# Kernel optimization log

Hardware: AMD Instinct MI355X
Metric: run time of the kernel (lower is better)

## Reference

```python
import jax, jax.numpy as jnp
import numpy as np


def _gru(x, w_ih, w_hh, b_ih, b_hh, reverse=False):
    # PyTorch GRU cell math. x: (N, T, Din) -> (N, T, Hh)
    N, T, _ = x.shape
    Hh = w_hh.shape[1]
    xp = jnp.einsum('ntd,gd->ntg', x, w_ih) + b_ih  # (N, T, 3*Hh), input gates precomputed

    def step(h, xp_t):
        gh = h @ w_hh.T + b_hh
        ir, iz, inn = jnp.split(xp_t, 3, axis=-1)
        hr, hz, hn = jnp.split(gh, 3, axis=-1)
        r = jax.nn.sigmoid(ir + hr)
        z = jax.nn.sigmoid(iz + hz)
        n = jnp.tanh(inn + r * hn)
        h_new = (1.0 - z) * n + z * h
        return h_new, h_new

    h0 = jnp.zeros((N, Hh), x.dtype)
    _, ys = jax.lax.scan(step, h0, jnp.swapaxes(xp, 0, 1), reverse=reverse)
    return jnp.swapaxes(ys, 0, 1)


def _bigru(x, pf, pb):
    return jnp.concatenate([_gru(x, *pf), _gru(x, *pb, reverse=True)], axis=-1)


def _attn(out, w, b, ctx):
    # out: (N, T, H). tanh(Linear) -> context dot -> softmax -> weighted sum
    u = jnp.tanh(jnp.einsum('nth,gh->ntg', out, w) + b)
    a = jax.nn.softmax(u @ ctx, axis=-1)  # (N, T)
    return jnp.einsum('nt,nth->nh', a, out)


def setup_inputs() -> dict:
    key = jax.random.key(0)
    H, Hh = 512, 256
    S, B, Nsent = 2048, 16, 16
    L = S // Nsent
    ks = jax.random.split(key, 32)

    def p(k, shape):
        return jax.random.normal(k, shape, jnp.float32) * 0.05

    starts = jnp.arange(Nsent, dtype=jnp.int32) * L
    spans = jnp.stack([starts, starts + L], axis=-1)  # (Nsent, 2)
    spans = jnp.broadcast_to(spans, (B, Nsent, 2))

    inp = {
        'token_feats': jax.random.normal(ks[0], (S, B, H), jnp.float32),
        'sentence_spans': spans,
        # word BiGRU params (forward / backward directions)
        'w_wih_f': p(ks[1], (3 * Hh, H)), 'w_whh_f': p(ks[2], (3 * Hh, Hh)),
        'w_bih_f': p(ks[3], (3 * Hh,)), 'w_bhh_f': p(ks[4], (3 * Hh,)),
        'w_wih_b': p(ks[5], (3 * Hh, H)), 'w_whh_b': p(ks[6], (3 * Hh, Hh)),
        'w_bih_b': p(ks[7], (3 * Hh,)), 'w_bhh_b': p(ks[8], (3 * Hh,)),
        # sentence BiGRU params
        's_wih_f': p(ks[9], (3 * Hh, H)), 's_whh_f': p(ks[10], (3 * Hh, Hh)),
        's_bih_f': p(ks[11], (3 * Hh,)), 's_bhh_f': p(ks[12], (3 * Hh,)),
        's_wih_b': p(ks[13], (3 * Hh, H)), 's_whh_b': p(ks[14], (3 * Hh, Hh)),
        's_bih_b': p(ks[15], (3 * Hh,)), 's_bhh_b': p(ks[16], (3 * Hh,)),
        # attention params
        'w_attn_w': p(ks[17], (H, H)), 'w_attn_b': p(ks[18], (H,)),
        'w_ctx': jax.random.normal(ks[19], (H,), jnp.float32),
        's_attn_w': p(ks[20], (H, H)), 's_attn_b': p(ks[21], (H,)),
        's_ctx': jax.random.normal(ks[22], (H,), jnp.float32),
    }
    return inp


def reference(token_feats, sentence_spans,
              w_wih_f, w_whh_f, w_bih_f, w_bhh_f,
              w_wih_b, w_whh_b, w_bih_b, w_bhh_b,
              s_wih_f, s_whh_f, s_bih_f, s_bhh_f,
              s_wih_b, s_whh_b, s_bih_b, s_bhh_b,
              w_attn_w, w_attn_b, w_ctx,
              s_attn_w, s_attn_b, s_ctx):
    S, B, H = token_feats.shape
    Nsent = sentence_spans.shape[1]
    L = S // Nsent  # uniform spans: segment b,i = tokens [i*L, (i+1)*L)

    x = jnp.swapaxes(token_feats, 0, 1)  # (B, S, H)
    segs = x.reshape(B * Nsent, L, H)    # all sentences batched together

    # word-level BiGRU + word attention -> sentence vectors
    out_w = _bigru(segs, (w_wih_f, w_whh_f, w_bih_f, w_bhh_f),
                   (w_wih_b, w_whh_b, w_bih_b, w_bhh_b))  # (B*Nsent, L, H)
    sent_vecs = _attn(out_w, w_attn_w, w_attn_b, w_ctx).reshape(B, Nsent, H)

    # sentence-level BiGRU + sentence attention (no padding: all masks true)
    out_s = _bigru(sent_vecs, (s_wih_f, s_whh_f, s_bih_f, s_bhh_f),
                   (s_wih_b, s_whh_b, s_bih_b, s_bhh_b))  # (B, Nsent, H)
    Yh = _attn(out_s, s_attn_w, s_attn_b, s_ctx)  # (B, H)
    return Yh
```

## Files before the change

kernel.cpp:

```cpp
#include <hip/hip_runtime.h>
#include <stdint.h>


using uint32  = unsigned int;
using bf16x8  = __attribute__((ext_vector_type(8))) __bf16;
using floatx4 = __attribute__((ext_vector_type(4))) float;

__device__ __forceinline__ float b2f(unsigned short u) {
    union { uint32 i; float f; } v; v.i = ((uint32)u) << 16; return v.f;
}
__device__ __forceinline__ unsigned short f2b(float f) {
    union { float f; uint32 i; } v; v.f = f;
    uint32 r = v.i + 0x7fffu + ((v.i >> 16) & 1u);
    return (unsigned short)(r >> 16);
}
__device__ __forceinline__ float sigmoidf_(float x) { return 1.f / (1.f + __expf(-x)); }
__device__ __forceinline__ float tanhf_(float x) {
    x = fminf(15.f, fmaxf(-15.f, x));
    float e = __expf(2.f * x);
    return (e - 1.f) / (e + 1.f);
}

__device__ __forceinline__ void gl16(const unsigned short* g, unsigned short* l) {
    __builtin_amdgcn_global_load_lds(
        (const __attribute__((address_space(1))) uint32*)g,
        (__attribute__((address_space(3))) uint32*)l, 16, 0, 0);
}

__device__ __forceinline__ void bar_lgkm() {
    asm volatile("s_waitcnt lgkmcnt(0)");
    __builtin_amdgcn_sched_barrier(0);
    __builtin_amdgcn_s_barrier();
    __builtin_amdgcn_sched_barrier(0);
}

#define O_XPC     0L
#define O_OWHI    50331648L
#define O_OWLO    83886080L
#define O_STATE   117440512L
#define O_SCW     117964800L
#define O_W0HI    118095872L
#define O_W0LO    118882304L
#define O_W1HI    119668736L
#define O_W1LO    120455168L
#define O_WAHI    121241600L
#define O_WALO    121765888L
#define O_S0HI    122290176L
#define O_S0LO    123076608L
#define O_S1HI    123863040L
#define O_S1LO    124649472L
#define O_SAHI    125435904L
#define O_SALO    125960192L
#define O_HW0     126484480L
#define O_HW1     126877696L
#define O_HS0     127270912L
#define O_HS1     127664128L
#define O_SENTHI  128057344L
#define O_SENTLO  128319488L
#define O_XPS     128581632L
#define O_SSTATE  130154496L
#define O_OSHI    130187264L
#define O_OSLO    130449408L
#define O_SCS     130711552L
#define O_TKWH    130712576L
#define O_TKWL    164267008L

__global__ __launch_bounds__(256)
void cvt_hilo6(const float* __restrict__ s0, const float* __restrict__ s1,
               const float* __restrict__ s2, const float* __restrict__ s3,
               const float* __restrict__ s4, const float* __restrict__ s5,
               char* __restrict__ ws)
{
    const int b = blockIdx.x;
    const float* src; unsigned short *hi, *lo; int base;
    if (b < 192)      { src = s0; hi = (unsigned short*)(ws + O_W0HI); lo = (unsigned short*)(ws + O_W0LO); base = b; }
    else if (b < 384) { src = s1; hi = (unsigned short*)(ws + O_W1HI); lo = (unsigned short*)(ws + O_W1LO); base = b - 192; }
    else if (b < 576) { src = s2; hi = (unsigned short*)(ws + O_S0HI); lo = (unsigned short*)(ws + O_S0LO); base = b - 384; }
    else if (b < 768) { src = s3; hi = (unsigned short*)(ws + O_S1HI); lo = (unsigned short*)(ws + O_S1LO); base = b - 576; }
    else if (b < 896) { src = s4; hi = (unsigned short*)(ws + O_WAHI); lo = (unsigned short*)(ws + O_WALO); base = b - 768; }
    else              { src = s5; hi = (unsigned short*)(ws + O_SAHI); lo = (unsigned short*)(ws + O_SALO); base = b - 896; }
    const int idx = (base * 256 + threadIdx.x) * 8;
    float f[8];
    *reinterpret_cast<float4*>(&f[0]) = *reinterpret_cast<const float4*>(src + idx);
    *reinterpret_cast<float4*>(&f[4]) = *reinterpret_cast<const float4*>(src + idx + 4);
    unsigned short h[8], l[8];
    #pragma unroll
    for (int j = 0; j < 8; ++j) {
        h[j] = f2b(f[j]);
        l[j] = f2b(f[j] - b2f(h[j]));
    }
    *reinterpret_cast<uint4*>(hi + idx) = *reinterpret_cast<const uint4*>(h);
    *reinterpret_cast<uint4*>(lo + idx) = *reinterpret_cast<const uint4*>(l);
}

__global__ __launch_bounds__(256)
void cvt_b4(const float* __restrict__ s0, const float* __restrict__ s1,
            const float* __restrict__ s2, const float* __restrict__ s3,
            char* __restrict__ ws)
{
    const int b = blockIdx.x;
    const float* src; unsigned short* dst; int base;
    if (b < 96)       { src = s0; dst = (unsigned short*)(ws + O_HW0); base = b; }
    else if (b < 192) { src = s1; dst = (unsigned short*)(ws + O_HW1); base = b - 96; }
    else if (b < 288) { src = s2; dst = (unsigned short*)(ws + O_HS0); base = b - 192; }
    else              { src = s3; dst = (unsigned short*)(ws + O_HS1); base = b - 288; }
    const int idx = (base * 256 + threadIdx.x) * 8;
    float f[8];
    *reinterpret_cast<float4*>(&f[0]) = *reinterpret_cast<const float4*>(src + idx);
    *reinterpret_cast<float4*>(&f[4]) = *reinterpret_cast<const float4*>(src + idx + 4);
    unsigned short o[8];
    #pragma unroll
    for (int j = 0; j < 8; ++j) o[j] = f2b(f[j]);
    *reinterpret_cast<uint4*>(dst + idx) = *reinterpret_cast<const uint4*>(o);
}

__global__ __launch_bounds__(256)
void cvt_tokfull(const float* __restrict__ tok, unsigned short* __restrict__ whi,
                 unsigned short* __restrict__ wlo)
{
    const int u = blockIdx.x * 256 + threadIdx.x;
    const int h8 = u & 63;
    const int rest = u >> 6;
    const int t = rest & 127, seq = rest >> 7;
    const int sent = seq & 15, b = seq >> 4;
    const long src = ((long)(sent * 128 + t) * 16 + b) * 512 + h8 * 8;
    float f[8];
    *reinterpret_cast<float4*>(&f[0]) = *reinterpret_cast<const float4*>(tok + src);
    *reinterpret_cast<float4*>(&f[4]) = *reinterpret_cast<const float4*>(tok + src + 4);
    unsigned short h[8], l[8];
    #pragma unroll
    for (int j = 0; j < 8; ++j) {
        h[j] = f2b(f[j]);
        l[j] = f2b(f[j] - b2f(h[j]));
    }
    const long dst = (long)rest * 512 + h8 * 8;
    *reinterpret_cast<uint4*>(whi + dst) = *reinterpret_cast<const uint4*>(h);
    *reinterpret_cast<uint4*>(wlo + dst) = *reinterpret_cast<const uint4*>(l);
}

template<int AMODE>
__device__ __forceinline__ long amap(int m, int t0, int sgn) {
    if (AMODE == 1) {
        const int sq = m >> 5, tl = m & 31;
        return (long)(sq * 128 + t0 + sgn * tl) * 512;
    } else if (AMODE == 3) {
        const int n = m >> 4, tl = m & 15;
        return (long)(n * 16 + t0 + sgn * tl) * 512;
    }
    return (long)m * 512;
}

template<int AMODE, int OUT>
__global__ __launch_bounds__(512, 2)
void gemm_t(const unsigned short* __restrict__ Ahi, const unsigned short* __restrict__ Alo,
            const unsigned short* __restrict__ Wh0, const unsigned short* __restrict__ Wl0,
            const unsigned short* __restrict__ Wh1, const unsigned short* __restrict__ Wl1,
            const float* __restrict__ b0, const float* __restrict__ b1,
            float* __restrict__ C, int ldC, long c1off,
            float* __restrict__ score, const float* __restrict__ ctx,
            int t00, int t01, int nbyHalf)
{
    __shared__ __align__(16) unsigned short smem[2 * 32768];

    int bx = blockIdx.x, by = blockIdx.y;
    {
        const int nbx = gridDim.x, nby = gridDim.y;
        if ((nby & 7) == 0) {
            const int l = by * nbx + bx;
            const int xcd = l & 7;
            const int s = l >> 3;
            bx = s % nbx;
            by = xcd * (nby >> 3) + s / nbx;
        }
    }

    const int tid  = threadIdx.x;
    const int lane = tid & 63;
    const int wave = tid >> 6;
    const int wm = wave >> 2, wn = wave & 3;
    const int n_base = bx * 256;
    const int q = lane >> 4;
    const int r = lane & 15;

    const unsigned short* Whi = Wh0;
    const unsigned short* Wlo = Wl0;
    const float* bias = b0;
    float* Cb = C;
    int t0 = t00, sgn = 1, m_base;
    if (nbyHalf > 0 && by >= nbyHalf) {
        Whi = Wh1; Wlo = Wl1; bias = b1; Cb = C + c1off;
        t0 = t01; sgn = -1;
        m_base = (by - nbyHalf) * 256;
    } else {
        m_base = by * 256;
    }

    long aoff[2], woff[2];
    #pragma unroll
    for (int i = 0; i < 2; ++i) {
        const int s = tid + 512 * i;
        const int R = s >> 2, kg = s & 3;
        const int kq = (kg - (R >> 1)) & 3;
        aoff[i] = amap<AMODE>(m_base + R, t0, sgn) + kq * 8;
        woff[i] = (long)(n_base + R) * 512 + kq * 8;
    }

    floatx4 acc[8][4];
    #pragma unroll
    for (int mt = 0; mt < 8; ++mt)
        #pragma unroll
        for (int nt = 0; nt < 4; ++nt) acc[mt][nt] = (floatx4){0.f, 0.f, 0.f, 0.f};

    auto stage = [&](int ts) {
        const int k0 = ts * 32;
        unsigned short* B = smem + (ts & 1) * 32768;
        #pragma unroll
        for (int i = 0; i < 2; ++i) {
            const int ld = (tid + 512 * i) * 8;
            gl16(Ahi + aoff[i] + k0, B + ld);
            gl16(Alo + aoff[i] + k0, B + 8192 + ld);
            gl16(Whi + woff[i] + k0, B + 16384 + ld);
            gl16(Wlo + woff[i] + k0, B + 24576 + ld);
        }
    };

    stage(0);
    asm volatile("s_waitcnt vmcnt(0)");
    __builtin_amdgcn_sched_barrier(0);
    __builtin_amdgcn_s_barrier();
    __builtin_amdgcn_sched_barrier(0);

    for (int t = 0; t < 16; ++t) {
        if (t + 1 < 16) stage(t + 1);

        const unsigned short* B   = smem + (t & 1) * 32768;
        const unsigned short* BAl = B + 8192;
        const unsigned short* BW  = B + 16384;
        const unsigned short* BWl = B + 24576;

        bf16x8 wh[4], wl[4], ah[8], al[8];
        #pragma unroll
        for (int nt = 0; nt < 4; ++nt) {
            const int Rn = wn * 64 + nt * 16 + r;
            const int sn = Rn * 4 + ((q + (Rn >> 1)) & 3);
            wh[nt] = *reinterpret_cast<const bf16x8*>(BW  + sn * 8);
            wl[nt] = *reinterpret_cast<const bf16x8*>(BWl + sn * 8);
        }
        #pragma unroll
        for (int mt = 0; mt < 8; ++mt) {
            const int R = wm * 128 + mt * 16 + r;
            const int s = R * 4 + ((q + (R >> 1)) & 3);
            ah[mt] = *reinterpret_cast<const bf16x8*>(B   + s * 8);
            al[mt] = *reinterpret_cast<const bf16x8*>(BAl + s * 8);
        }
        asm volatile("s_waitcnt lgkmcnt(0)");
        __builtin_amdgcn_sched_barrier(0);

        #pragma unroll
        for (int mt = 0; mt < 8; ++mt)
            #pragma unroll
            for (int nt = 0; nt < 4; ++nt) {
                acc[mt][nt] = __builtin_amdgcn_mfma_f32_16x16x32_bf16(ah[mt], wh[nt], acc[mt][nt], 0, 0, 0);
                acc[mt][nt] = __builtin_amdgcn_mfma_f32_16x16x32_bf16(ah[mt], wl[nt], acc[mt][nt], 0, 0, 0);
                acc[mt][nt] = __builtin_amdgcn_mfma_f32_16x16x32_bf16(al[mt], wh[nt], acc[mt][nt], 0, 0, 0);
            }

        __builtin_amdgcn_sched_barrier(0);
        asm volatile("s_waitcnt vmcnt(0)");
        __builtin_amdgcn_sched_barrier(0);
        __builtin_amdgcn_s_barrier();
        __builtin_amdgcn_sched_barrier(0);
    }

    if (OUT == 0) {
        #pragma unroll
        for (int nt = 0; nt < 4; ++nt) {
            const int n = n_base + wn * 64 + nt * 16 + r;
            const float bs = bias[n];
            #pragma unroll
            for (int mt = 0; mt < 8; ++mt) {
                const int m = m_base + wm * 128 + mt * 16 + q * 4;
                #pragma unroll
                for (int e = 0; e < 4; ++e)
                    Cb[(long)(m + e) * ldC + n] = acc[mt][nt][e] + bs;
            }
        }
    } else {
        #pragma unroll
        for (int mt = 0; mt < 8; ++mt) {
            float p[4] = {0.f, 0.f, 0.f, 0.f};
            #pragma unroll
            for (int nt = 0; nt < 4; ++nt) {
                const int n = n_base + wn * 64 + nt * 16 + r;
                const float cx = ctx[n];
                const float bs = bias[n];
                #pragma unroll
                for (int e = 0; e < 4; ++e)
                    p[e] += cx * tanhf_(acc[mt][nt][e] + bs);
            }
            #pragma unroll
            for (int mk = 1; mk < 16; mk <<= 1) {
                #pragma unroll
                for (int e = 0; e < 4; ++e) p[e] += __shfl_xor(p[e], mk, 64);
            }
            if (r == 0) {
                const int m = m_base + wm * 128 + mt * 16 + q * 4;
                #pragma unroll
                for (int e = 0; e < 4; ++e)
                    atomicAdd(&score[m + e], p[e]);
            }
        }
    }
}

template<int AMODE, int OUT>
__global__ __launch_bounds__(256)
void gemm_d(const unsigned short* __restrict__ Ahi, const unsigned short* __restrict__ Alo,
            const unsigned short* __restrict__ Wh0, const unsigned short* __restrict__ Wl0,
            const unsigned short* __restrict__ Wh1, const unsigned short* __restrict__ Wl1,
            const float* __restrict__ b0, const float* __restrict__ b1,
            float* __restrict__ C, int ldC, long c1off,
            float* __restrict__ score, const float* __restrict__ ctx,
            int t00, int t01, int nbyHalf)
{
    __shared__ __align__(16) unsigned short smem[2 * 16384];

    int bx = blockIdx.x, by = blockIdx.y;
    {
        const int nbx = gridDim.x, nby = gridDim.y;
        if ((nby & 7) == 0) {
            const int l = by * nbx + bx;
            const int xcd = l & 7;
            const int s = l >> 3;
            bx = s % nbx;
            by = xcd * (nby >> 3) + s / nbx;
        }
    }

    const int tid  = threadIdx.x;
    const int lane = tid & 63;
    const int wave = tid >> 6;
    const int wm = wave >> 1, wn = wave & 1;
    const int n_base = bx * 128;
    const int q = lane >> 4;
    const int r = lane & 15;

    const unsigned short* Whi = Wh0;
    const unsigned short* Wlo = Wl0;
    const float* bias = b0;
    float* Cb = C;
    int t0 = t00, sgn = 1, m_base;
    if (nbyHalf > 0 && by >= nbyHalf) {
        Whi = Wh1; Wlo = Wl1; bias = b1; Cb = C + c1off;
        t0 = t01; sgn = -1;
        m_base = (by - nbyHalf) * 128;
    } else {
        m_base = by * 128;
    }

    long aoff[2], woff[2];
    #pragma unroll
    for (int i = 0; i < 2; ++i) {
        const int s = tid + 256 * i;
        const int R = s >> 2, kg = s & 3;
        const int kq = (kg - (R >> 1)) & 3;
        aoff[i] = amap<AMODE>(m_base + R, t0, sgn) + kq * 8;
        woff[i] = (long)(n_base + R) * 512 + kq * 8;
    }

    floatx4 acc[4][4];
    #pragma unroll
    for (int mt = 0; mt < 4; ++mt)
        #pragma unroll
        for (int nt = 0; nt < 4; ++nt) acc[mt][nt] = (floatx4){0.f, 0.f, 0.f, 0.f};

    auto stage = [&](int ts) {
        const int k0 = ts * 32;
        unsigned short* B = smem + (ts & 1) * 16384;
        #pragma unroll
        for (int i = 0; i < 2; ++i) {
            const int ld = (tid + 256 * i) * 8;
            gl16(Ahi + aoff[i] + k0, B + ld);
            gl16(Alo + aoff[i] + k0, B + 4096 + ld);
            gl16(Whi + woff[i] + k0, B + 8192 + ld);
            gl16(Wlo + woff[i] + k0, B + 12288 + ld);
        }
    };

    stage(0);
    for (int t = 0; t < 16; ++t) {
        stage(t + 1 < 16 ? t + 1 : 15);
        asm volatile("s_waitcnt vmcnt(8)\n\ts_barrier" ::: "memory");

        const unsigned short* B = smem + (t & 1) * 16384;
        bf16x8 ah[4], al[4];
        #pragma unroll
        for (int mt = 0; mt < 4; ++mt) {
            const int R = wm * 64 + mt * 16 + r;
            const int s = R * 4 + ((q + (R >> 1)) & 3);
            ah[mt] = *reinterpret_cast<const bf16x8*>(B + s * 8);
            al[mt] = *reinterpret_cast<const bf16x8*>(B + 4096 + s * 8);
        }
        #pragma unroll
        for (int nt = 0; nt < 4; ++nt) {
            const int Rn = wn * 64 + nt * 16 + r;
            const int sn = Rn * 4 + ((q + (Rn >> 1)) & 3);
            bf16x8 wh = *reinterpret_cast<const bf16x8*>(B + 8192 + sn * 8);
            bf16x8 wl = *reinterpret_cast<const bf16x8*>(B + 12288 + sn * 8);
            #pragma unroll
            for (int mt = 0; mt < 4; ++mt) {
                acc[mt][nt] = __builtin_amdgcn_mfma_f32_16x16x32_bf16(ah[mt], wh, acc[mt][nt], 0, 0, 0);
                acc[mt][nt] = __builtin_amdgcn_mfma_f32_16x16x32_bf16(ah[mt], wl, acc[mt][nt], 0, 0, 0);
                acc[mt][nt] = __builtin_amdgcn_mfma_f32_16x16x32_bf16(al[mt], wh, acc[mt][nt], 0, 0, 0);
            }
        }
        asm volatile("s_waitcnt lgkmcnt(0)\n\ts_barrier" ::: "memory");
    }
    asm volatile("s_waitcnt vmcnt(0)" ::: "memory");

    if (OUT == 0) {
        #pragma unroll
        for (int nt = 0; nt < 4; ++nt) {
            const int n = n_base + wn * 64 + nt * 16 + r;
            const float bs = bias[n];
            #pragma unroll
            for (int mt = 0; mt < 4; ++mt) {
                const int m = m_base + wm * 64 + mt * 16 + q * 4;
                #pragma unroll
                for (int e = 0; e < 4; ++e)
                    Cb[(long)(m + e) * ldC + n] = acc[mt][nt][e] + bs;
            }
        }
    } else {
        #pragma unroll
        for (int mt = 0; mt < 4; ++mt) {
            float p[4] = {0.f, 0.f, 0.f, 0.f};
            #pragma unroll
            for (int nt = 0; nt < 4; ++nt) {
                const int n = n_base + wn * 64 + nt * 16 + r;
                const float cx = ctx[n];
                const float bs = bias[n];
                #pragma unroll
                for (int e = 0; e < 4; ++e)
                    p[e] += cx * tanhf_(acc[mt][nt][e] + bs);
            }
            #pragma unroll
            for (int mk = 1; mk < 16; mk <<= 1) {
                #pragma unroll
                for (int e = 0; e < 4; ++e) p[e] += __shfl_xor(p[e], mk, 64);
            }
            if (r == 0) {
                const int m = m_base + wm * 64 + mt * 16 + q * 4;
                #pragma unroll
                for (int e = 0; e < 4; ++e)
                    atomicAdd(&score[m + e], p[e]);
            }
        }
    }
}

__global__ __launch_bounds__(512, 2)
void gru2(const float* __restrict__ xp,
          const unsigned short* __restrict__ Wf,
          const unsigned short* __restrict__ Wb,
          const float* __restrict__ bhf, const float* __restrict__ bhb,
          float* __restrict__ state,
          unsigned short* __restrict__ ohi, unsigned short* __restrict__ olo,
          int steps, int t0f, int t0b, int groups, int Tout)
{
    __shared__ float pre[768 * 5];
    __shared__ unsigned short Bf[8 * 64 * 8];

    const int tid  = threadIdx.x;
    const int lane = tid & 63;
    const int w    = tid >> 6;
    const int dir  = blockIdx.x / groups;
    const int g    = blockIdx.x % groups;
    const int nseq = groups * 2;
    const unsigned short* W = dir ? Wb : Wf;
    const float* bh = dir ? bhb : bhf;
    const int t0  = dir ? t0b : t0f;
    const int sgn = dir ? -1 : 1;

    const int s = tid >> 8;
    const int j = tid & 255;
    const float bhr = bh[j], bhz = bh[j + 256], bhn = bh[j + 512];

    bf16x8 wf[6][8];
    {
        const int r0 = w * 96 + (lane & 15);
        const int kf = (lane >> 4) * 8;
        #pragma unroll
        for (int mt = 0; mt < 6; ++mt)
            #pragma unroll
            for (int kk = 0; kk < 8; ++kk)
                wf[mt][kk] = *reinterpret_cast<const bf16x8*>(
                    W + (long)(r0 + mt * 16) * 256 + kk * 32 + kf);
    }

    #pragma unroll
    for (int i = 0; i < 4; ++i)
        reinterpret_cast<uint32*>(Bf)[tid * 4 + i] = 0;

    float h = state[((long)dir * nseq + g * 2 + s) * 256 + j];
    const int posHi = ((j >> 5) * 64 + ((j >> 3) & 3) * 16 + s) * 8 + (j & 7);
    const int posLo = ((j >> 5) * 64 + ((j >> 3) & 3) * 16 + 2 + s) * 8 + (j & 7);
    {
        const unsigned short hb = f2b(h);
        Bf[posHi] = hb;
        Bf[posLo] = f2b(h - b2f(hb));
    }
    bar_lgkm();

    const float* xbase = xp + (long)dir * nseq * steps * 768
                       + (long)(g * 2 + s) * steps * 768;
    const int q = lane >> 4, r = lane & 15;

    float xr = xbase[j], xz = xbase[256 + j], xn = xbase[512 + j];

    for (int st = 0; st < steps; ++st) {
        const int t = t0 + sgn * st;

        const int sn = (st + 1 < steps) ? st + 1 : st;
        const float* xb = xbase + (long)sn * 768;
        const float nxr = xb[j];
        const float nxz = xb[256 + j];
        const float nxn = xb[512 + j];

        floatx4 acc[6];
        #pragma unroll
        for (int mt = 0; mt < 6; ++mt) acc[mt] = (floatx4){0.f, 0.f, 0.f, 0.f};
        #pragma unroll
        for (int kk = 0; kk < 8; ++kk) {
            bf16x8 bv = *reinterpret_cast<const bf16x8*>(Bf + (kk * 64 + lane) * 8);
            #pragma unroll
            for (int mt = 0; mt < 6; ++mt)
                acc[mt] = __builtin_amdgcn_mfma_f32_16x16x32_bf16(wf[mt][kk], bv, acc[mt], 0, 0, 0);
        }
        if (r < 4) {
            #pragma unroll
            for (int mt = 0; mt < 6; ++mt) {
                const int row = w * 96 + mt * 16 + q * 4;
                #pragma unroll
                for (int e = 0; e < 4; ++e)
                    pre[(row + e) * 5 + r] = acc[mt][e];
            }
        }
        bar_lgkm();

        {
            const float pr = pre[j * 5 + s]         + pre[j * 5 + 2 + s];
            const float pz = pre[(j + 256) * 5 + s] + pre[(j + 256) * 5 + 2 + s];
            const float pn = pre[(j + 512) * 5 + s] + pre[(j + 512) * 5 + 2 + s];
            const float rg = sigmoidf_(xr + pr + bhr);
            const float zg = sigmoidf_(xz + pz + bhz);
            const float nn = tanhf_(xn + rg * (pn + bhn));
            h = (1.f - zg) * nn + zg * h;
            const unsigned short hb = f2b(h);
            const unsigned short lb = f2b(h - b2f(hb));
            Bf[posHi] = hb;
            Bf[posLo] = lb;
            const long orow = ((long)(g * 2 + s) * Tout + t) * 512 + dir * 256 + j;
            ohi[orow] = hb;
            olo[orow] = lb;
        }
        xr = nxr; xz = nxz; xn = nxn;
        bar_lgkm();
    }

    state[((long)dir * nseq + g * 2 + s) * 256 + j] = h;
}

template<int MODE, int T>
__global__ __launch_bounds__(256)
void attn_wsum(const float* __restrict__ score,
               const unsigned short* __restrict__ fhi,
               const unsigned short* __restrict__ flo,
               void* __restrict__ o1, void* __restrict__ o2)
{
    const int n = blockIdx.x;
    const int tid = threadIdx.x;
    __shared__ float a[T];
    __shared__ float e[T];
    if (tid < T) a[tid] = score[n * T + tid];
    __syncthreads();
    float mx = -1e30f;
    #pragma unroll
    for (int t = 0; t < T; ++t) mx = fmaxf(mx, a[t]);
    if (tid < T) e[tid] = __expf(a[tid] - mx);
    __syncthreads();
    float sm = 0.f;
    #pragma unroll
    for (int t = 0; t < T; ++t) sm += e[t];
    const float inv = 1.f / sm;
    float acc0 = 0.f, acc1 = 0.f;
    #pragma unroll 8
    for (int t = 0; t < T; ++t) {
        const float w = e[t] * inv;
        const long base = ((long)n * T + t) * 512;
        acc0 += w * (b2f(fhi[base + tid])       + b2f(flo[base + tid]));
        acc1 += w * (b2f(fhi[base + tid + 256]) + b2f(flo[base + tid + 256]));
    }
    if (MODE == 1) {
        float* o = (float*)o1;
        o[n * 512 + tid] = acc0;
        o[n * 512 + tid + 256] = acc1;
    } else {
        unsigned short* oh = (unsigned short*)o1;
        unsigned short* ol = (unsigned short*)o2;
        const unsigned short h0 = f2b(acc0), h1 = f2b(acc1);
        oh[n * 512 + tid]       = h0;  ol[n * 512 + tid]       = f2b(acc0 - b2f(h0));
        oh[n * 512 + tid + 256] = h1;  ol[n * 512 + tid + 256] = f2b(acc1 - b2f(h1));
    }
}

extern "C" void kernel_launch(void* const* d_in, const int* in_sizes, int n_in,
                              void* d_out, int out_size, void* d_ws, size_t ws_size,
                              hipStream_t stream) {
    const float* tok      = (const float*)d_in[0];
    const float* w_wih_f  = (const float*)d_in[2];
    const float* w_whh_f  = (const float*)d_in[3];
    const float* w_bih_f  = (const float*)d_in[4];
    const float* w_bhh_f  = (const float*)d_in[5];
    const float* w_wih_b  = (const float*)d_in[6];
    const float* w_whh_b  = (const float*)d_in[7];
    const float* w_bih_b  = (const float*)d_in[8];
    const float* w_bhh_b  = (const float*)d_in[9];
    const float* s_wih_f  = (const float*)d_in[10];
    const float* s_whh_f  = (const float*)d_in[11];
    const float* s_bih_f  = (const float*)d_in[12];
    const float* s_bhh_f  = (const float*)d_in[13];
    const float* s_wih_b  = (const float*)d_in[14];
    const float* s_whh_b  = (const float*)d_in[15];
    const float* s_bih_b  = (const float*)d_in[16];
    const float* s_bhh_b  = (const float*)d_in[17];
    const float* w_attn_b = (const float*)d_in[19];
    const float* w_ctx    = (const float*)d_in[20];
    const float* s_attn_b = (const float*)d_in[22];
    const float* s_ctx    = (const float*)d_in[23];

    char* ws = (char*)d_ws;
    float*          xpc   = (float*)(ws + O_XPC);
    unsigned short* owhi  = (unsigned short*)(ws + O_OWHI);
    unsigned short* owlo  = (unsigned short*)(ws + O_OWLO);
    float*          state = (float*)(ws + O_STATE);
    float*          score_w = (float*)(ws + O_SCW);
    unsigned short* W0HI  = (unsigned short*)(ws + O_W0HI);
    unsigned short* W0LO  = (unsigned short*)(ws + O_W0LO);
    unsigned short* W1HI  = (unsigned short*)(ws + O_W1HI);
    unsigned short* W1LO  = (unsigned short*)(ws + O_W1LO);
    unsigned short* WAHI  = (unsigned short*)(ws + O_WAHI);
    unsigned short* WALO  = (unsigned short*)(ws + O_WALO);
    unsigned short* S0HI  = (unsigned short*)(ws + O_S0HI);
    unsigned short* S0LO  = (unsigned short*)(ws + O_S0LO);
    unsigned short* S1HI  = (unsigned short*)(ws + O_S1HI);
    unsigned short* S1LO  = (unsigned short*)(ws + O_S1LO);
    unsigned short* SAHI  = (unsigned short*)(ws + O_SAHI);
    unsigned short* SALO  = (unsigned short*)(ws + O_SALO);
    unsigned short* HW0   = (unsigned short*)(ws + O_HW0);
    unsigned short* HW1   = (unsigned short*)(ws + O_HW1);
    unsigned short* HS0   = (unsigned short*)(ws + O_HS0);
    unsigned short* HS1   = (unsigned short*)(ws + O_HS1);
    unsigned short* senthi = (unsigned short*)(ws + O_SENTHI);
    unsigned short* sentlo = (unsigned short*)(ws + O_SENTLO);
    float*          xp_s  = (float*)(ws + O_XPS);
    float*          sstate = (float*)(ws + O_SSTATE);
    unsigned short* oshi  = (unsigned short*)(ws + O_OSHI);
    unsigned short* oslo  = (unsigned short*)(ws + O_OSLO);
    float*          score_s = (float*)(ws + O_SCS);
    unsigned short* tkwh  = (unsigned short*)(ws + O_TKWH);
    unsigned short* tkwl  = (unsigned short*)(ws + O_TKWL);

    const dim3 blk(256);

    hipMemsetAsync(ws + O_STATE,  0, 524288, stream);
    hipMemsetAsync(ws + O_SSTATE, 0, 32768, stream);
    hipMemsetAsync(ws + O_SCW,    0, 131072, stream);
    hipMemsetAsync(ws + O_SCS,    0, 1024, stream);

    cvt_hilo6<<<dim3(1024), blk, 0, stream>>>(w_wih_f, w_wih_b, s_wih_f, s_wih_b,
                                              (const float*)d_in[18], (const float*)d_in[21], ws);
    cvt_b4<<<dim3(384), blk, 0, stream>>>(w_whh_f, w_whh_b, s_whh_f, s_whh_b, ws);
    cvt_tokfull<<<dim3(8192), blk, 0, stream>>>(tok, tkwh, tkwl);

    const long XDW = 256L * 32 * 768;
    for (int c = 0; c < 4; ++c) {
        gemm_t<1, 0><<<dim3(3, 64), dim3(512), 0, stream>>>(
            tkwh, tkwl, W0HI, W0LO, W1HI, W1LO, w_bih_f, w_bih_b,
            xpc, 768, XDW, nullptr, nullptr, 32 * c, 127 - 32 * c, 32);
        gru2<<<dim3(256), dim3(512), 0, stream>>>(
            xpc, HW0, HW1, w_bhh_f, w_bhh_b, state, owhi, owlo,
            32, 32 * c, 127 - 32 * c, 128, 128);
    }

    gemm_t<2, 1><<<dim3(2, 128), dim3(512), 0, stream>>>(
        owhi, owlo, WAHI, WALO, WAHI, WALO, w_attn_b, w_attn_b,
        nullptr, 0, 0, score_w, w_ctx, 0, 0, 0);
    attn_wsum<0, 128><<<dim3(256), blk, 0, stream>>>(score_w, owhi, owlo, senthi, sentlo);

    const long XDS = 16L * 16 * 768;
    gemm_d<3, 0><<<dim3(6, 4), blk, 0, stream>>>(
        senthi, sentlo, S0HI, S0LO, S1HI, S1LO, s_bih_f, s_bih_b,
        xp_s, 768, XDS, nullptr, nullptr, 0, 15, 2);

    gru2<<<dim3(16), dim3(512), 0, stream>>>(
        xp_s, HS0, HS1, s_bhh_f, s_bhh_b, sstate, oshi, oslo,
        16, 0, 15, 8, 16);

    gemm_d<2, 1><<<dim3(4, 2), blk, 0, stream>>>(
        oshi, oslo, SAHI, SALO, SAHI, SALO, s_attn_b, s_attn_b,
        nullptr, 0, 0, score_s, s_ctx, 0, 0, 0);
    attn_wsum<1, 16><<<dim3(16), blk, 0, stream>>>(score_s, oshi, oslo, d_out, nullptr);
}
```

Before: 693.4 us.

## Remap GRU recurrence rows per wave and double-buffer hidden state to drop barrier

The recurrent GRU kernel now assigns each wave the r/z/n gate rows for its own 32 hidden units. Each wave can then read its MFMA results back from a wave-private shared buffer, so the block-wide barrier between the matmul and the gate update becomes a wave-local lgkmcnt wait. The hidden-state operand buffer is double-buffered so that writes for the next step do not race with reads of the current step, leaving one barrier per step instead of two. Threads are remapped so adjacent lanes hold the two sequences, which makes output stores less coalesced.

```diff
diff --git a/kernel.cpp b/kernel.cpp
--- a/kernel.cpp
+++ b/kernel.cpp
@@ -468,8 +468,8 @@
           unsigned short* __restrict__ ohi, unsigned short* __restrict__ olo,
           int steps, int t0f, int t0b, int groups, int Tout)
 {
-    __shared__ float pre[768 * 5];
-    __shared__ unsigned short Bf[8 * 64 * 8];
+    __shared__ float preS[8][6][16][4];
+    __shared__ unsigned short Bf[2][4096];
 
     const int tid  = threadIdx.x;
     const int lane = tid & 63;
@@ -482,85 +482,97 @@
     const int t0  = dir ? t0b : t0f;
     const int sgn = dir ? -1 : 1;
 
-    const int s = tid >> 8;
-    const int j = tid & 255;
-    const float bhr = bh[j], bhz = bh[j + 256], bhn = bh[j + 512];
+    const int s  = lane & 1;
+    const int lr = lane >> 1;
+    const int u  = w * 32 + lr;
+
+    const float bhr = bh[u], bhz = bh[u + 256], bhn = bh[u + 512];
 
     bf16x8 wf[6][8];
     {
-        const int r0 = w * 96 + (lane & 15);
+        const int rl = lane & 15;
         const int kf = (lane >> 4) * 8;
         #pragma unroll
-        for (int mt = 0; mt < 6; ++mt)
+        for (int mt = 0; mt < 6; ++mt) {
+            const int R = (mt >> 1) * 256 + w * 32 + (mt & 1) * 16 + rl;
             #pragma unroll
             for (int kk = 0; kk < 8; ++kk)
                 wf[mt][kk] = *reinterpret_cast<const bf16x8*>(
-                    W + (long)(r0 + mt * 16) * 256 + kk * 32 + kf);
-    }
-
-    #pragma unroll
-    for (int i = 0; i < 4; ++i)
-        reinterpret_cast<uint32*>(Bf)[tid * 4 + i] = 0;
-
-    float h = state[((long)dir * nseq + g * 2 + s) * 256 + j];
-    const int posHi = ((j >> 5) * 64 + ((j >> 3) & 3) * 16 + s) * 8 + (j & 7);
-    const int posLo = ((j >> 5) * 64 + ((j >> 3) & 3) * 16 + 2 + s) * 8 + (j & 7);
+                    W + (long)R * 256 + kk * 32 + kf);
+        }
+    }
+
+    #pragma unroll
+    for (int i = 0; i < 8; ++i)
+        reinterpret_cast<uint32*>(Bf)[tid * 8 + i] = 0;
+
+    float h = state[((long)dir * nseq + g * 2 + s) * 256 + u];
+    const int bposHi = (w * 64 + (lr >> 3) * 16 + s) * 8 + (lr & 7);
+    const int bposLo = (w * 64 + (lr >> 3) * 16 + 2 + s) * 8 + (lr & 7);
     {
         const unsigned short hb = f2b(h);
-        Bf[posHi] = hb;
-        Bf[posLo] = f2b(h - b2f(hb));
+        Bf[0][bposHi] = hb;
+        Bf[0][bposLo] = f2b(h - b2f(hb));
     }
     bar_lgkm();
 
     const float* xbase = xp + (long)dir * nseq * steps * 768
                        + (long)(g * 2 + s) * steps * 768;
-    const int q = lane >> 4, r = lane & 15;
-
-    float xr = xbase[j], xz = xbase[256 + j], xn = xbase[512 + j];
+
+    float xr = xbase[u], xz = xbase[256 + u], xn = xbase[512 + u];
+
+    const int c  = lane & 15;
+    const int q  = lane >> 4;
+    const int rit  = lr & 15;
+    const int hsel = lr >> 4;
 
     for (int st = 0; st < steps; ++st) {
         const int t = t0 + sgn * st;
-
-        const int sn = (st + 1 < steps) ? st + 1 : st;
-        const float* xb = xbase + (long)sn * 768;
-        const float nxr = xb[j];
-        const float nxz = xb[256 + j];
-        const float nxn = xb[512 + j];
+        const int cur = st & 1;
+
+        const int sn2 = (st + 1 < steps) ? st + 1 : st;
+        const float* xb = xbase + (long)sn2 * 768;
+        const float nxr = xb[u];
+        const float nxz = xb[256 + u];
+        const float nxn = xb[512 + u];
 
         floatx4 acc[6];
         #pragma unroll
         for (int mt = 0; mt < 6; ++mt) acc[mt] = (floatx4){0.f, 0.f, 0.f, 0.f};
         #pragma unroll
         for (int kk = 0; kk < 8; ++kk) {
-            bf16x8 bv = *reinterpret_cast<const bf16x8*>(Bf + (kk * 64 + lane) * 8);
+            bf16x8 bv = *reinterpret_cast<const bf16x8*>(&Bf[cur][(kk * 64 + lane) * 8]);
             #pragma unroll
             for (int mt = 0; mt < 6; ++mt)
                 acc[mt] = __builtin_amdgcn_mfma_f32_16x16x32_bf16(wf[mt][kk], bv, acc[mt], 0, 0, 0);
         }
-        if (r < 4) {
-            #pragma unroll
-            for (int mt = 0; mt < 6; ++mt) {
-                const int row = w * 96 + mt * 16 + q * 4;
+
+        if (c < 4) {
+            #pragma unroll
+            for (int mt = 0; mt < 6; ++mt)
                 #pragma unroll
                 for (int e = 0; e < 4; ++e)
-                    pre[(row + e) * 5 + r] = acc[mt][e];
-            }
-        }
-        bar_lgkm();
+                    preS[w][mt][q * 4 + e][c] = acc[mt][e];
+        }
+        asm volatile("s_waitcnt lgkmcnt(0)");
+        __builtin_amdgcn_sched_barrier(0);
 
         {
-            const float pr = pre[j * 5 + s]         + pre[j * 5 + 2 + s];
-            const float pz = pre[(j + 256) * 5 + s] + pre[(j + 256) * 5 + 2 + s];
-            const float pn = pre[(j + 512) * 5 + s] + pre[(j + 512) * 5 + 2 + s];
+            const float4 fr = *reinterpret_cast<const float4*>(&preS[w][0 + hsel][rit][0]);
+            const float4 fz = *reinterpret_cast<const float4*>(&preS[w][2 + hsel][rit][0]);
+            const float4 fn = *reinterpret_cast<const float4*>(&preS[w][4 + hsel][rit][0]);
+            const float pr = (s ? fr.y : fr.x) + (s ? fr.w : fr.z);
+            const float pz = (s ? fz.y : fz.x) + (s ? fz.w : fz.z);
+            const float pn = (s ? fn.y : fn.x) + (s ? fn.w : fn.z);
             const float rg = sigmoidf_(xr + pr + bhr);
             const float zg = sigmoidf_(xz + pz + bhz);
             const float nn = tanhf_(xn + rg * (pn + bhn));
             h = (1.f - zg) * nn + zg * h;
             const unsigned short hb = f2b(h);
             const unsigned short lb = f2b(h - b2f(hb));
-            Bf[posHi] = hb;
-            Bf[posLo] = lb;
-            const long orow = ((long)(g * 2 + s) * Tout + t) * 512 + dir * 256 + j;
+            Bf[cur ^ 1][bposHi] = hb;
+            Bf[cur ^ 1][bposLo] = lb;
+            const long orow = ((long)(g * 2 + s) * Tout + t) * 512 + dir * 256 + u;
             ohi[orow] = hb;
             olo[orow] = lb;
         }
@@ -568,7 +580,7 @@
         bar_lgkm();
     }
 
-    state[((long)dir * nseq + g * 2 + s) * 256 + j] = h;
+    state[((long)dir * nseq + g * 2 + s) * 256 + u] = h;
 }
 
 template<int MODE, int T>
```

Measured after the change: 678.1 us. 2.2% less time.
